# Optimization experiments

Hardware: AMD Instinct MI355X
Metric: run time of the kernel (lower is better)

Reference implementation:

```python
import jax, jax.numpy as jnp
import numpy as np

K = 16          # num_bins
BOUND = 5.0     # tail_bound
MBW = 1e-3      # min_bin_width
MBH = 1e-3      # min_bin_height
MD = 1e-3       # min_derivative


def setup_inputs() -> dict:
    key = jax.random.key(0)
    ks = jax.random.split(key, 6)
    B, N, CD, H = 4096, 1024, 64, 256
    OUT = 3 * K + 1  # 2K widths/heights + (K+1) derivatives

    def lin_w(k, fan_in, shape):
        return (jax.random.normal(k, shape, jnp.float32) / np.sqrt(fan_in)).astype(jnp.float32)

    return {
        "cond": jax.random.normal(ks[0], (B, CD), jnp.float32),
        "y": jax.random.normal(ks[1], (B, N), jnp.float32) * 2.0,
        "W1": lin_w(ks[2], CD, (CD, H)), "b1": jnp.zeros((H,), jnp.float32),
        "W2": lin_w(ks[3], H, (H, H)),   "b2": jnp.zeros((H,), jnp.float32),
        "W3": lin_w(ks[4], H, (H, OUT)), "b3": jnp.zeros((OUT,), jnp.float32),
    }


def reference(cond, y, W1, b1, W2, b2, W3, b3):
    # --- conditioner MLP (concat mode, depth=2, dropout=0 / eval) ---
    h = jax.nn.relu(cond @ W1 + b1)
    h = jax.nn.relu(h @ W2 + b2)
    p = h @ W3 + b3                      # (B, 3K+1)
    un_w, un_h, un_d = p[..., :K], p[..., K:2 * K], p[..., 2 * K:]

    left, right, bottom, top = -BOUND, BOUND, -BOUND, BOUND
    widths = MBW + (right - left - K * MBW) * jax.nn.softmax(un_w, axis=-1)    # (B, K)
    heights = MBH + (top - bottom - K * MBH) * jax.nn.softmax(un_h, axis=-1)   # (B, K)
    cumw = jnp.pad(jnp.cumsum(widths, axis=-1), ((0, 0), (1, 0))) + left       # (B, K+1)
    cumh = jnp.pad(jnp.cumsum(heights, axis=-1), ((0, 0), (1, 0))) + bottom    # (B, K+1)
    deriv = MD + jax.nn.softplus(un_d)                                         # (B, K+1)

    xc = jnp.clip(y, left, right)                                              # (B, N)
    # bin search: O(K) broadcasted compare+sum, as in the original
    bin_idx = jnp.sum(xc[..., None] >= cumw[:, None, 1:], axis=-1)             # (B, N) int
    bin_idx = jnp.clip(bin_idx, 0, K - 1)

    gat = lambda a, i: jnp.take_along_axis(a, i, axis=-1)  # (B,K')[(B,N)] -> (B,N)
    x0 = gat(cumw, bin_idx)
    w = gat(widths, bin_idx)
    y0 = gat(cumh, bin_idx)
    hh = gat(heights, bin_idx)
    d0 = gat(deriv, bin_idx)
    d1 = gat(deriv, bin_idx + 1)

    delta = hh / w
    theta = (xc - x0) / w
    omt = 1.0 - theta
    num = hh * (delta * theta * theta + d0 * theta * omt)
    den = delta + (d0 + d1 - 2.0 * delta) * theta * omt
    out = y0 + num / den

    der_num = jnp.maximum(delta * delta * (d1 * theta * theta + 2.0 * delta * theta * omt + d0 * omt * omt), 1e-12)
    der_den = jnp.maximum(den * den, 1e-12)
    logdet = jnp.log(der_num) - jnp.log(der_den)

    outside = (y < left) | (y > right)
    out = jnp.where(outside, y, out)
    logdet = jnp.where(outside, jnp.zeros_like(logdet), logdet)
    return out, logdet
```

## Files before the change

### kernel.cpp

```cpp
#include <hip/hip_runtime.h>
#include <math.h>

namespace {
constexpr int KB    = 16;
constexpr int OUTP  = 3*KB + 1;
constexpr int CDIM  = 64;
constexpr int HDIM  = 256;
constexpr int NCOL  = 1024;
constexpr int NROW  = 4096;
constexpr float BOUNDF = 5.0f;
constexpr float MBW_ = 0.001f;
constexpr float MBH_ = 0.001f;
constexpr float MD_  = 0.001f;
constexpr int NR   = 8;
}

__global__ __launch_bounds__(256, 2) void fused_spline_flow_kernel(
    const float* __restrict__ cond,
    const float* __restrict__ y,
    const float* __restrict__ W1, const float* __restrict__ b1,
    const float* __restrict__ W2, const float* __restrict__ b2,
    const float* __restrict__ W3, const float* __restrict__ b3,
    float* __restrict__ out, float* __restrict__ logdet)
{
    __shared__ float cond_s[NR][CDIM];
    __shared__ float ps[4][NR][HDIM];
    __shared__ float h_s[NR][HDIM];
    __shared__ float p_s[NR][OUTP];
    __shared__ float prm_s[NR][51];
    __shared__ float scan_s[NR][16];
    __shared__ float rec[NR][KB][8];

    const int tid  = threadIdx.x;
    const int lane = tid & 63;
    const int wid  = tid >> 6;
    const int row0 = blockIdx.x * NR;

    if (tid < NR*CDIM/4)
        *((float4*)&cond_s[0][0] + tid) = *((const float4*)(cond + (size_t)row0*CDIM) + tid);
    __syncthreads();

    {
        float acc[NR][4];
        #pragma unroll
        for (int r = 0; r < NR; ++r)
            #pragma unroll
            for (int c = 0; c < 4; ++c) acc[r][c] = 0.f;

        #pragma unroll
        for (int kg = 0; kg < 4; ++kg) {
            const int k0 = 16*wid + 4*kg;
            float4 wv[4];
            #pragma unroll
            for (int kk = 0; kk < 4; ++kk)
                wv[kk] = *(const float4*)(W1 + (size_t)(k0+kk)*HDIM + 4*lane);
            #pragma unroll
            for (int r = 0; r < NR; ++r) {
                const float4 cv4 = *(const float4*)&cond_s[r][k0];
                const float cv[4] = {cv4.x, cv4.y, cv4.z, cv4.w};
                const float wf[4][4] = {{wv[0].x,wv[0].y,wv[0].z,wv[0].w},
                                        {wv[1].x,wv[1].y,wv[1].z,wv[1].w},
                                        {wv[2].x,wv[2].y,wv[2].z,wv[2].w},
                                        {wv[3].x,wv[3].y,wv[3].z,wv[3].w}};
                #pragma unroll
                for (int kk = 0; kk < 4; ++kk)
                    #pragma unroll
                    for (int c = 0; c < 4; ++c)
                        acc[r][c] = fmaf(cv[kk], wf[kk][c], acc[r][c]);
            }
        }
        #pragma unroll
        for (int r = 0; r < NR; ++r)
            *(float4*)&ps[wid][r][4*lane] = make_float4(acc[r][0], acc[r][1], acc[r][2], acc[r][3]);
    }
    __syncthreads();
    {
        const float bb = b1[tid];
        #pragma unroll
        for (int r = 0; r < NR; ++r)
            h_s[r][tid] = fmaxf(ps[0][r][tid] + ps[1][r][tid] + ps[2][r][tid] + ps[3][r][tid] + bb, 0.f);
    }
    __syncthreads();

    {
        float acc[NR][4];
        #pragma unroll
        for (int r = 0; r < NR; ++r)
            #pragma unroll
            for (int c = 0; c < 4; ++c) acc[r][c] = 0.f;

        float4 wn[4];
        #pragma unroll
        for (int kk = 0; kk < 4; ++kk)
            wn[kk] = *(const float4*)(W2 + (size_t)(64*wid+kk)*HDIM + 4*lane);

        #pragma unroll 2
        for (int kg = 0; kg < 16; ++kg) {
            const int k0 = 64*wid + 4*kg;
            float4 wv[4];
            #pragma unroll
            for (int kk = 0; kk < 4; ++kk) wv[kk] = wn[kk];
            if (kg < 15) {
                #pragma unroll
                for (int kk = 0; kk < 4; ++kk)
                    wn[kk] = *(const float4*)(W2 + (size_t)(k0+4+kk)*HDIM + 4*lane);
            }
            #pragma unroll
            for (int r = 0; r < NR; ++r) {
                const float4 hv4 = *(const float4*)&h_s[r][k0];
                const float hv[4] = {hv4.x, hv4.y, hv4.z, hv4.w};
                const float wf[4][4] = {{wv[0].x,wv[0].y,wv[0].z,wv[0].w},
                                        {wv[1].x,wv[1].y,wv[1].z,wv[1].w},
                                        {wv[2].x,wv[2].y,wv[2].z,wv[2].w},
                                        {wv[3].x,wv[3].y,wv[3].z,wv[3].w}};
                #pragma unroll
                for (int kk = 0; kk < 4; ++kk)
                    #pragma unroll
                    for (int c = 0; c < 4; ++c)
                        acc[r][c] = fmaf(hv[kk], wf[kk][c], acc[r][c]);
            }
        }
        #pragma unroll
        for (int r = 0; r < NR; ++r)
            *(float4*)&ps[wid][r][4*lane] = make_float4(acc[r][0], acc[r][1], acc[r][2], acc[r][3]);
    }
    __syncthreads();
    {
        const float bb = b2[tid];
        #pragma unroll
        for (int r = 0; r < NR; ++r)
            h_s[r][tid] = fmaxf(ps[0][r][tid] + ps[1][r][tid] + ps[2][r][tid] + ps[3][r][tid] + bb, 0.f);
    }
    __syncthreads();

    {
        const int  o   = lane;
        const bool act = (o < OUTP);
        float acc[NR];
        #pragma unroll
        for (int r = 0; r < NR; ++r) acc[r] = 0.f;

        #pragma unroll 4
        for (int kg = 0; kg < 16; ++kg) {
            const int k0 = 64*wid + 4*kg;
            float wv[4];
            #pragma unroll
            for (int kk = 0; kk < 4; ++kk)
                wv[kk] = act ? W3[(size_t)(k0+kk)*OUTP + o] : 0.f;
            #pragma unroll
            for (int r = 0; r < NR; ++r) {
                const float4 hv = *(const float4*)&h_s[r][k0];
                acc[r] = fmaf(hv.x, wv[0], acc[r]);
                acc[r] = fmaf(hv.y, wv[1], acc[r]);
                acc[r] = fmaf(hv.z, wv[2], acc[r]);
                acc[r] = fmaf(hv.w, wv[3], acc[r]);
            }
        }
        if (act) {
            #pragma unroll
            for (int r = 0; r < NR; ++r) ps[wid][r][o] = acc[r];
        }
    }
    __syncthreads();
    for (int t = tid; t < NR*OUTP; t += 256) {
        const int r = t / OUTP;
        const int o = t - r*OUTP;
        p_s[r][o] = ps[0][r][o] + ps[1][r][o] + ps[2][r][o] + ps[3][r][o] + b3[o];
    }
    __syncthreads();

    if (tid < NR*3) {
        const int r   = tid / 3;
        const int seg = tid - 3*r;
        if (seg < 2) {
            const int   off   = (seg == 0) ? 0 : KB;
            const int   cbase = (seg == 0) ? 0 : 17;
            const float mb    = (seg == 0) ? MBW_ : MBH_;
            float m = -1e30f;
            #pragma unroll
            for (int i = 0; i < KB; ++i) m = fmaxf(m, p_s[r][off+i]);
            float e[KB];
            float s = 0.f;
            #pragma unroll
            for (int i = 0; i < KB; ++i) { e[i] = __expf(p_s[r][off+i] - m); s += e[i]; }
            const float span = (2.f*BOUNDF - (float)KB*mb) / s;
            float c = -BOUNDF;
            prm_s[r][cbase] = c;
            #pragma unroll
            for (int i = 0; i < KB; ++i) {
                c += mb + span*e[i];
                prm_s[r][cbase + 1 + i] = c;
            }
        } else {
            #pragma unroll
            for (int i = 0; i < KB+1; ++i) {
                const float x  = p_s[r][2*KB + i];
                const float sp = (x > 20.f) ? x : __logf(1.f + __expf(x));
                prm_s[r][34 + i] = MD_ + sp;
            }
        }
    }
    __syncthreads();

    if (tid < NR*KB) {
        const int r = tid >> 4;
        const int k = tid & 15;
        rec[r][k][0] = prm_s[r][k];
        rec[r][k][1] = prm_s[r][k+1];
        rec[r][k][2] = prm_s[r][17+k];
        rec[r][k][3] = prm_s[r][17+k+1];
        rec[r][k][4] = prm_s[r][34+k];
        rec[r][k][5] = prm_s[r][34+k+1];
        rec[r][k][6] = 0.f; rec[r][k][7] = 0.f;
        scan_s[r][k] = prm_s[r][k+1];
    }
    __syncthreads();

    float4 yv[NR];
    #pragma unroll
    for (int e = 0; e < NR; ++e)
        yv[e] = *(const float4*)(y + (size_t)(row0+e)*NCOL + 4*tid);

    #pragma unroll 2
    for (int e = 0; e < NR; ++e) {
        float cw[KB];
        #pragma unroll
        for (int q = 0; q < 4; ++q) {
            const float4 t4 = *(const float4*)&scan_s[e][4*q];
            cw[4*q+0] = t4.x; cw[4*q+1] = t4.y; cw[4*q+2] = t4.z; cw[4*q+3] = t4.w;
        }
        const float yy[4] = {yv[e].x, yv[e].y, yv[e].z, yv[e].w};
        float ov[4], lv[4];
        #pragma unroll
        for (int i = 0; i < 4; ++i) {
            const float yi = yy[i];
            const bool outside = (yi < -BOUNDF) || (yi > BOUNDF);
            const float xc = fminf(fmaxf(yi, -BOUNDF), BOUNDF);
            int bin = 0;
            #pragma unroll
            for (int k = 0; k < KB; ++k) bin += (xc >= cw[k]) ? 1 : 0;
            bin = min(bin, KB-1);

            const float4 lo = *(const float4*)&rec[e][bin][0];
            const float2 hi = *(const float2*)&rec[e][bin][4];
            const float w  = lo.y - lo.x;
            const float hh = lo.w - lo.z;
            const float d0 = hi.x, d1 = hi.y;

            const float inv_w = __fdividef(1.f, w);
            const float delta = hh * inv_w;
            const float theta = (xc - lo.x) * inv_w;
            const float omt   = 1.f - theta;
            const float tt    = theta * theta;
            const float tomt  = theta * omt;
            const float num   = hh * (delta*tt + d0*tomt);
            const float den   = delta + (d0 + d1 - 2.f*delta)*tomt;
            const float o     = lo.z + __fdividef(num, den);
            const float der_num = fmaxf(delta*delta*(d1*tt + 2.f*delta*tomt + d0*omt*omt), 1e-12f);
            const float der_den = fmaxf(den*den, 1e-12f);
            const float ld      = __logf(__fdividef(der_num, der_den));

            ov[i] = outside ? yi : o;
            lv[i] = outside ? 0.f : ld;
        }
        const size_t base = (size_t)(row0+e) * NCOL + 4*tid;
        *(float4*)(out + base)    = make_float4(ov[0], ov[1], ov[2], ov[3]);
        *(float4*)(logdet + base) = make_float4(lv[0], lv[1], lv[2], lv[3]);
    }
}

extern "C" void kernel_launch(void* const* d_in, const int* in_sizes, int n_in,
                              void* d_out, int out_size, void* d_ws, size_t ws_size,
                              hipStream_t stream) {
    const float* cond = (const float*)d_in[0];
    const float* y    = (const float*)d_in[1];
    const float* W1   = (const float*)d_in[2];
    const float* b1   = (const float*)d_in[3];
    const float* W2   = (const float*)d_in[4];
    const float* b2   = (const float*)d_in[5];
    const float* W3   = (const float*)d_in[6];
    const float* b3   = (const float*)d_in[7];

    float* out    = (float*)d_out;
    float* logdet = out + (size_t)NROW * NCOL;

    fused_spline_flow_kernel<<<NROW/NR, 256, 0, stream>>>(
        cond, y, W1, b1, W2, b2, W3, b3, out, logdet);
}
```

Measured before the change: 43.29 us.

## Split fused kernel into MLP-parameter kernel and per-row spline kernel

Separates the conditioner MLP from the spline evaluation into two launches that exchange the 51 per-row spline parameters through the workspace buffer. The spline kernel now uses one block per row (4096 blocks) instead of eight rows per block, so the memory-streaming phase gets more parallelism and is not serialized behind the MLP inside each block. In exchange it adds a second launch, a global round trip for the parameters, and loses any overlap between MLP compute and y streaming within a fused block.

```diff
diff --git a/kernel.cpp b/kernel.cpp
--- a/kernel.cpp
+++ b/kernel.cpp
@@ -12,24 +12,22 @@
 constexpr float MBW_ = 0.001f;
 constexpr float MBH_ = 0.001f;
 constexpr float MD_  = 0.001f;
+constexpr int PSTR = 51;
 constexpr int NR   = 8;
 }
 
-__global__ __launch_bounds__(256, 2) void fused_spline_flow_kernel(
+__global__ __launch_bounds__(256) void mlp_params_kernel(
     const float* __restrict__ cond,
-    const float* __restrict__ y,
     const float* __restrict__ W1, const float* __restrict__ b1,
     const float* __restrict__ W2, const float* __restrict__ b2,
     const float* __restrict__ W3, const float* __restrict__ b3,
-    float* __restrict__ out, float* __restrict__ logdet)
+    float* __restrict__ params)
 {
     __shared__ float cond_s[NR][CDIM];
     __shared__ float ps[4][NR][HDIM];
     __shared__ float h_s[NR][HDIM];
     __shared__ float p_s[NR][OUTP];
-    __shared__ float prm_s[NR][51];
-    __shared__ float scan_s[NR][16];
-    __shared__ float rec[NR][KB][8];
+    __shared__ float prm_s[NR][PSTR];
 
     const int tid  = threadIdx.x;
     const int lane = tid & 63;
@@ -202,71 +200,81 @@
     }
     __syncthreads();
 
-    if (tid < NR*KB) {
-        const int r = tid >> 4;
-        const int k = tid & 15;
-        rec[r][k][0] = prm_s[r][k];
-        rec[r][k][1] = prm_s[r][k+1];
-        rec[r][k][2] = prm_s[r][17+k];
-        rec[r][k][3] = prm_s[r][17+k+1];
-        rec[r][k][4] = prm_s[r][34+k];
-        rec[r][k][5] = prm_s[r][34+k+1];
-        rec[r][k][6] = 0.f; rec[r][k][7] = 0.f;
-        scan_s[r][k] = prm_s[r][k+1];
-    }
-    __syncthreads();
-
-    float4 yv[NR];
+    for (int i = tid; i < NR*PSTR; i += 256)
+        params[(size_t)row0*PSTR + i] = (&prm_s[0][0])[i];
+}
+
+__global__ __launch_bounds__(256) void spline_kernel(
+    const float* __restrict__ y,
+    const float* __restrict__ params,
+    float* __restrict__ out,
+    float* __restrict__ logdet)
+{
+    __shared__ float prm[PSTR];
+    __shared__ float rec[KB][8];
+    __shared__ float scan_s[KB];
+
+    const int b   = blockIdx.x;
+    const int tid = threadIdx.x;
+    if (tid < PSTR) prm[tid] = params[(size_t)b*PSTR + tid];
+    __syncthreads();
+    if (tid < KB) {
+        const int k = tid;
+        rec[k][0] = prm[k];        rec[k][1] = prm[k+1];
+        rec[k][2] = prm[17+k];     rec[k][3] = prm[17+k+1];
+        rec[k][4] = prm[34+k];     rec[k][5] = prm[34+k+1];
+        rec[k][6] = 0.f;           rec[k][7] = 0.f;
+        scan_s[k] = prm[k+1];
+    }
+    __syncthreads();
+
+    float cw[KB];
     #pragma unroll
-    for (int e = 0; e < NR; ++e)
-        yv[e] = *(const float4*)(y + (size_t)(row0+e)*NCOL + 4*tid);
-
-    #pragma unroll 2
-    for (int e = 0; e < NR; ++e) {
-        float cw[KB];
-        #pragma unroll
-        for (int q = 0; q < 4; ++q) {
-            const float4 t4 = *(const float4*)&scan_s[e][4*q];
-            cw[4*q+0] = t4.x; cw[4*q+1] = t4.y; cw[4*q+2] = t4.z; cw[4*q+3] = t4.w;
-        }
-        const float yy[4] = {yv[e].x, yv[e].y, yv[e].z, yv[e].w};
-        float ov[4], lv[4];
-        #pragma unroll
-        for (int i = 0; i < 4; ++i) {
-            const float yi = yy[i];
-            const bool outside = (yi < -BOUNDF) || (yi > BOUNDF);
-            const float xc = fminf(fmaxf(yi, -BOUNDF), BOUNDF);
-            int bin = 0;
-            #pragma unroll
-            for (int k = 0; k < KB; ++k) bin += (xc >= cw[k]) ? 1 : 0;
-            bin = min(bin, KB-1);
-
-            const float4 lo = *(const float4*)&rec[e][bin][0];
-            const float2 hi = *(const float2*)&rec[e][bin][4];
-            const float w  = lo.y - lo.x;
-            const float hh = lo.w - lo.z;
-            const float d0 = hi.x, d1 = hi.y;
-
-            const float inv_w = __fdividef(1.f, w);
-            const float delta = hh * inv_w;
-            const float theta = (xc - lo.x) * inv_w;
-            const float omt   = 1.f - theta;
-            const float tt    = theta * theta;
-            const float tomt  = theta * omt;
-            const float num   = hh * (delta*tt + d0*tomt);
-            const float den   = delta + (d0 + d1 - 2.f*delta)*tomt;
-            const float o     = lo.z + __fdividef(num, den);
-            const float der_num = fmaxf(delta*delta*(d1*tt + 2.f*delta*tomt + d0*omt*omt), 1e-12f);
-            const float der_den = fmaxf(den*den, 1e-12f);
-            const float ld      = __logf(__fdividef(der_num, der_den));
-
-            ov[i] = outside ? yi : o;
-            lv[i] = outside ? 0.f : ld;
-        }
-        const size_t base = (size_t)(row0+e) * NCOL + 4*tid;
-        *(float4*)(out + base)    = make_float4(ov[0], ov[1], ov[2], ov[3]);
-        *(float4*)(logdet + base) = make_float4(lv[0], lv[1], lv[2], lv[3]);
-    }
+    for (int q = 0; q < 4; ++q) {
+        const float4 t4 = *(const float4*)&scan_s[4*q];
+        cw[4*q+0] = t4.x; cw[4*q+1] = t4.y; cw[4*q+2] = t4.z; cw[4*q+3] = t4.w;
+    }
+
+    const size_t base = (size_t)b * NCOL + 4*tid;
+    const float4 yv   = *(const float4*)(y + base);
+    const float  yy[4] = {yv.x, yv.y, yv.z, yv.w};
+    float ov[4], lv[4];
+
+    #pragma unroll
+    for (int i = 0; i < 4; ++i) {
+        const float yi = yy[i];
+        const bool outside = (yi < -BOUNDF) || (yi > BOUNDF);
+        const float xc = fminf(fmaxf(yi, -BOUNDF), BOUNDF);
+        int bin = 0;
+        #pragma unroll
+        for (int k = 0; k < KB; ++k) bin += (xc >= cw[k]) ? 1 : 0;
+        bin = min(bin, KB-1);
+
+        const float4 lo = *(const float4*)&rec[bin][0];
+        const float2 hi = *(const float2*)&rec[bin][4];
+        const float w  = lo.y - lo.x;
+        const float hh = lo.w - lo.z;
+        const float d0 = hi.x, d1 = hi.y;
+
+        const float inv_w = __fdividef(1.f, w);
+        const float delta = hh * inv_w;
+        const float theta = (xc - lo.x) * inv_w;
+        const float omt   = 1.f - theta;
+        const float tt    = theta * theta;
+        const float tomt  = theta * omt;
+        const float num   = hh * (delta*tt + d0*tomt);
+        const float den   = delta + (d0 + d1 - 2.f*delta)*tomt;
+        const float o     = lo.z + __fdividef(num, den);
+        const float der_num = fmaxf(delta*delta*(d1*tt + 2.f*delta*tomt + d0*omt*omt), 1e-12f);
+        const float der_den = fmaxf(den*den, 1e-12f);
+        const float ld      = __logf(__fdividef(der_num, der_den));
+
+        ov[i] = outside ? yi : o;
+        lv[i] = outside ? 0.f : ld;
+    }
+
+    *(float4*)(out + base)    = make_float4(ov[0], ov[1], ov[2], ov[3]);
+    *(float4*)(logdet + base) = make_float4(lv[0], lv[1], lv[2], lv[3]);
 }
 
 extern "C" void kernel_launch(void* const* d_in, const int* in_sizes, int n_in,
@@ -283,7 +291,8 @@
 
     float* out    = (float*)d_out;
     float* logdet = out + (size_t)NROW * NCOL;
-
-    fused_spline_flow_kernel<<<NROW/NR, 256, 0, stream>>>(
-        cond, y, W1, b1, W2, b2, W3, b3, out, logdet);
-}
+    float* params = (float*)d_ws;
+
+    mlp_params_kernel<<<NROW/NR, 256, 0, stream>>>(cond, W1, b1, W2, b2, W3, b3, params);
+    spline_kernel<<<NROW, 256, 0, stream>>>(y, params, out, logdet);
+}
```

Measured after the change: 38.02 us. -12.2%, faster.
